# Performance work log

Measured on AMD Instinct MI355X. Metric: run time of the kernel, lower is better.

## Reference

```python
import jax, jax.numpy as jnp
import numpy as np

N, D, K = 262144, 64, 512


def setup_inputs() -> dict:
    key = jax.random.key(0)
    k1, k2 = jax.random.split(key)
    x = jax.random.normal(k1, (N, D), dtype=jnp.float32)
    # embedding initialized uniform(-1/K, 1/K) as in the torch module
    codebook = jax.random.uniform(k2, (K, D), dtype=jnp.float32, minval=-1.0 / K, maxval=1.0 / K)
    return {"x": x, "codebook": codebook}


def reference(x, codebook):
    # distances[n,k] = ||x_n||^2 + ||w_k||^2 - 2 x_n . w_k  (cdist^2 via matmul)
    d = (jnp.sum(x * x, axis=1, keepdims=True)
         + jnp.sum(codebook * codebook, axis=1)
         - 2.0 * jnp.matmul(x, codebook.T))  # [N, K]
    indices = jnp.argmin(d, axis=1)          # [N]
    x_q = codebook[indices]                  # [N, D] gather
    commitment_loss = jnp.mean((jax.lax.stop_gradient(x_q) - x) ** 2)
    embedding_loss = jnp.mean((x_q - jax.lax.stop_gradient(x)) ** 2)
    vq_loss = commitment_loss * 0.25 + embedding_loss
    # straight-through estimator
    x_out = x + jax.lax.stop_gradient(x_q - x)
    return (x_out, vq_loss)
```

## Files before the change

### kernel.cpp

```cpp
#include <hip/hip_runtime.h>
#include <hip/hip_bf16.h>

#define N_ROWS 262144
#define DIM    64
#define KCB    512

#define BLOCKS  512
#define THREADS 512

typedef __bf16 bf16x8 __attribute__((ext_vector_type(8)));
typedef float  f32x4  __attribute__((ext_vector_type(4)));

__device__ inline float dot4(float4 a) {
    return a.x * a.x + a.y * a.y + a.z * a.z + a.w * a.w;
}

__global__ void vq_wnorm(const float* __restrict__ cb, float* __restrict__ wn) {
    int k = threadIdx.x;
    if (k < KCB) {
        const float* w = cb + k * DIM;
        float s = 0.f;
        #pragma unroll
        for (int d = 0; d < DIM; ++d) s += w[d] * w[d];
        wn[k] = 1.0f + 0.5f * s;
    }
}

__global__ __launch_bounds__(THREADS, 4) void vq_main(
    const float* __restrict__ x, const float* __restrict__ cb,
    const float* __restrict__ wn, float* __restrict__ out,
    float* __restrict__ partials)
{
    __shared__ bf16x8 cb_sh[KCB * 8];
    __shared__ f32x4  wn_sh4[KCB / 4];
    __shared__ float  red_sh[THREADS];

    const int tid    = threadIdx.x;
    const int lane   = tid & 63;
    const int wave   = tid >> 6;
    const int lane15 = lane & 15;
    const int half   = lane >> 4;

    for (int fg = tid; fg < KCB * 8; fg += THREADS) {
        int row = fg >> 3, g = fg & 7;
        const float* src = cb + row * DIM + g * 8;
        float4 f0 = *(const float4*)src;
        float4 f1 = *(const float4*)(src + 4);
        bf16x8 v;
        v[0] = (__bf16)(-f0.x); v[1] = (__bf16)(-f0.y); v[2] = (__bf16)(-f0.z); v[3] = (__bf16)(-f0.w);
        v[4] = (__bf16)(-f1.x); v[5] = (__bf16)(-f1.y); v[6] = (__bf16)(-f1.z); v[7] = (__bf16)(-f1.w);
        cb_sh[row * 8 + (g ^ (row & 7))] = v;
    }
    for (int i = tid; i < KCB; i += THREADS) ((float*)wn_sh4)[i] = wn[i];

    const int wrow = blockIdx.x * (8 * 64) + wave * 64;
    bf16x8 blo[4], bhi[4];
    float  xn[4];
    #pragma unroll
    for (int c = 0; c < 4; ++c) {
        const float* xr = x + (size_t)(wrow + c * 16 + lane15) * DIM + half * 8;
        float4 f0 = *(const float4*)xr;
        float4 f1 = *(const float4*)(xr + 4);
        float4 f2 = *(const float4*)(xr + 32);
        float4 f3 = *(const float4*)(xr + 36);
        xn[c] = dot4(f0) + dot4(f1) + dot4(f2) + dot4(f3);
        bf16x8 lo, hi;
        lo[0] = (__bf16)f0.x; lo[1] = (__bf16)f0.y; lo[2] = (__bf16)f0.z; lo[3] = (__bf16)f0.w;
        lo[4] = (__bf16)f1.x; lo[5] = (__bf16)f1.y; lo[6] = (__bf16)f1.z; lo[7] = (__bf16)f1.w;
        hi[0] = (__bf16)f2.x; hi[1] = (__bf16)f2.y; hi[2] = (__bf16)f2.z; hi[3] = (__bf16)f2.w;
        hi[4] = (__bf16)f3.x; hi[5] = (__bf16)f3.y; hi[6] = (__bf16)f3.z; hi[7] = (__bf16)f3.w;
        blo[c] = lo; bhi[c] = hi;
    }
    __syncthreads();

    const int swz_lo = half ^ (lane & 7);
    const int swz_hi = (4 + half) ^ (lane & 7);
    const unsigned halfbits = (unsigned)(half * 4);

    unsigned u0 = 0xFFFFFFFFu, u1 = 0xFFFFFFFFu, u2 = 0xFFFFFFFFu, u3 = 0xFFFFFFFFu;

    #pragma unroll 8
    for (int t = 0; t < 32; ++t) {
        const int arow = t * 16 + lane15;
        bf16x8 alo = cb_sh[arow * 8 + swz_lo];
        bf16x8 ahi = cb_sh[arow * 8 + swz_hi];
        f32x4  wnv = wn_sh4[t * 4 + half];
        unsigned* us[4] = {&u0, &u1, &u2, &u3};
        #pragma unroll
        for (int c = 0; c < 4; ++c) {
            f32x4 acc = wnv;
            acc = __builtin_amdgcn_mfma_f32_16x16x32_bf16(alo, blo[c], acc, 0, 0, 0);
            acc = __builtin_amdgcn_mfma_f32_16x16x32_bf16(ahi, bhi[c], acc, 0, 0, 0);
            unsigned p0 = (__float_as_uint(acc[0]) & 0xFFFFFE00u) | (unsigned)(t * 16 + 0) | halfbits;
            unsigned p1 = (__float_as_uint(acc[1]) & 0xFFFFFE00u) | (unsigned)(t * 16 + 1) | halfbits;
            unsigned p2 = (__float_as_uint(acc[2]) & 0xFFFFFE00u) | (unsigned)(t * 16 + 2) | halfbits;
            unsigned p3 = (__float_as_uint(acc[3]) & 0xFFFFFE00u) | (unsigned)(t * 16 + 3) | halfbits;
            unsigned a = p0 < p1 ? p0 : p1;
            unsigned b = p2 < p3 ? p2 : p3;
            unsigned m = a < b ? a : b;
            *us[c] = (*us[c] < m) ? *us[c] : m;
        }
    }

    float lossAcc = 0.f;
    int bks[4];
    unsigned uc[4] = {u0, u1, u2, u3};
    #pragma unroll
    for (int c = 0; c < 4; ++c) {
        unsigned v = uc[c];
        unsigned w16 = (unsigned)__shfl_xor((int)v, 16); v = v < w16 ? v : w16;
        unsigned w32 = (unsigned)__shfl_xor((int)v, 32); v = v < w32 ? v : w32;
        float xnf = xn[c];
        xnf += __shfl_xor(xnf, 16);
        xnf += __shfl_xor(xnf, 32);
        bks[c] = (int)(v & 511u);
        float sstar = __uint_as_float(v & 0xFFFFFE00u);
        lossAcc += 0.25f * (xnf + 2.f * (sstar - 1.f));
    }

    float* outw = out + (size_t)wrow * DIM;
    #pragma unroll
    for (int j = 0; j < 16; ++j) {
        int srcl = (j * 4 + half) & 15;
        int bk   = __shfl(bks[j >> 2], srcl);
        float4 q = *(const float4*)(cb + (size_t)bk * DIM + (lane & 15) * 4);
        *(float4*)(outw + j * 256 + lane * 4) = q;
    }

    red_sh[tid] = lossAcc;
    __syncthreads();
    #pragma unroll
    for (int s = THREADS / 2; s > 0; s >>= 1) {
        if (tid < s) red_sh[tid] += red_sh[tid + s];
        __syncthreads();
    }
    if (tid == 0) partials[blockIdx.x] = red_sh[0];
}

__global__ void vq_finalize(const float* __restrict__ partials,
                            float* __restrict__ out_loss) {
    __shared__ float sh[256];
    int t = threadIdx.x;
    sh[t] = partials[t] + partials[t + 256];
    __syncthreads();
    #pragma unroll
    for (int s = 128; s > 0; s >>= 1) {
        if (t < s) sh[t] += sh[t + s];
        __syncthreads();
    }
    if (t == 0) out_loss[0] = sh[0] * (1.25f / (float)(N_ROWS * DIM));
}

extern "C" void kernel_launch(void* const* d_in, const int* in_sizes, int n_in,
                              void* d_out, int out_size, void* d_ws, size_t ws_size,
                              hipStream_t stream) {
    const float* x  = (const float*)d_in[0];
    const float* cb = (const float*)d_in[1];
    float* out      = (float*)d_out;
    float* wn       = (float*)d_ws;
    float* partials = wn + KCB;

    hipLaunchKernelGGL(vq_wnorm, dim3(1), dim3(512), 0, stream, cb, wn);
    hipLaunchKernelGGL(vq_main, dim3(BLOCKS), dim3(THREADS), 0, stream,
                       x, cb, wn, out, partials);
    hipLaunchKernelGGL(vq_finalize, dim3(1), dim3(256), 0, stream,
                       partials, out + (size_t)N_ROWS * DIM);
}
```

Baseline: 45.74 us.

## Fuse codebook norm into main kernel, double threads per block, use shuffle reductions

```diff
diff --git a/kernel.cpp b/kernel.cpp
--- a/kernel.cpp
+++ b/kernel.cpp
@@ -6,7 +6,7 @@
 #define KCB    512
 
 #define BLOCKS  512
-#define THREADS 512
+#define THREADS 1024
 
 typedef __bf16 bf16x8 __attribute__((ext_vector_type(8)));
 typedef float  f32x4  __attribute__((ext_vector_type(4)));
@@ -15,25 +15,13 @@
     return a.x * a.x + a.y * a.y + a.z * a.z + a.w * a.w;
 }
 
-__global__ void vq_wnorm(const float* __restrict__ cb, float* __restrict__ wn) {
-    int k = threadIdx.x;
-    if (k < KCB) {
-        const float* w = cb + k * DIM;
-        float s = 0.f;
-        #pragma unroll
-        for (int d = 0; d < DIM; ++d) s += w[d] * w[d];
-        wn[k] = 1.0f + 0.5f * s;
-    }
-}
-
-__global__ __launch_bounds__(THREADS, 4) void vq_main(
+__global__ __launch_bounds__(THREADS, 8) void vq_main(
     const float* __restrict__ x, const float* __restrict__ cb,
-    const float* __restrict__ wn, float* __restrict__ out,
-    float* __restrict__ partials)
+    float* __restrict__ out, float* __restrict__ partials)
 {
     __shared__ bf16x8 cb_sh[KCB * 8];
     __shared__ f32x4  wn_sh4[KCB / 4];
-    __shared__ float  red_sh[THREADS];
+    __shared__ float  red_sh[16];
 
     const int tid    = threadIdx.x;
     const int lane   = tid & 63;
@@ -41,23 +29,29 @@
     const int lane15 = lane & 15;
     const int half   = lane >> 4;
 
-    for (int fg = tid; fg < KCB * 8; fg += THREADS) {
-        int row = fg >> 3, g = fg & 7;
+    #pragma unroll
+    for (int it = 0; it < (KCB * 8) / THREADS; ++it) {
+        const int fg = tid + it * THREADS;
+        const int row = fg >> 3, g = fg & 7;
         const float* src = cb + row * DIM + g * 8;
         float4 f0 = *(const float4*)src;
         float4 f1 = *(const float4*)(src + 4);
+        float sq = dot4(f0) + dot4(f1);
+        sq += __shfl_xor(sq, 1);
+        sq += __shfl_xor(sq, 2);
+        sq += __shfl_xor(sq, 4);
         bf16x8 v;
         v[0] = (__bf16)(-f0.x); v[1] = (__bf16)(-f0.y); v[2] = (__bf16)(-f0.z); v[3] = (__bf16)(-f0.w);
         v[4] = (__bf16)(-f1.x); v[5] = (__bf16)(-f1.y); v[6] = (__bf16)(-f1.z); v[7] = (__bf16)(-f1.w);
         cb_sh[row * 8 + (g ^ (row & 7))] = v;
+        if (g == 0) ((float*)wn_sh4)[row] = 1.0f + 0.5f * sq;
     }
-    for (int i = tid; i < KCB; i += THREADS) ((float*)wn_sh4)[i] = wn[i];
 
-    const int wrow = blockIdx.x * (8 * 64) + wave * 64;
-    bf16x8 blo[4], bhi[4];
-    float  xn[4];
+    const int wrow = blockIdx.x * 512 + wave * 32;
+    bf16x8 blo[2], bhi[2];
+    float  xn[2];
     #pragma unroll
-    for (int c = 0; c < 4; ++c) {
+    for (int c = 0; c < 2; ++c) {
         const float* xr = x + (size_t)(wrow + c * 16 + lane15) * DIM + half * 8;
         float4 f0 = *(const float4*)xr;
         float4 f1 = *(const float4*)(xr + 4);
@@ -77,7 +71,7 @@
     const int swz_hi = (4 + half) ^ (lane & 7);
     const unsigned halfbits = (unsigned)(half * 4);
 
-    unsigned u0 = 0xFFFFFFFFu, u1 = 0xFFFFFFFFu, u2 = 0xFFFFFFFFu, u3 = 0xFFFFFFFFu;
+    unsigned u0 = 0xFFFFFFFFu, u1 = 0xFFFFFFFFu;
 
     #pragma unroll 8
     for (int t = 0; t < 32; ++t) {
@@ -85,9 +79,9 @@
         bf16x8 alo = cb_sh[arow * 8 + swz_lo];
         bf16x8 ahi = cb_sh[arow * 8 + swz_hi];
         f32x4  wnv = wn_sh4[t * 4 + half];
-        unsigned* us[4] = {&u0, &u1, &u2, &u3};
+        unsigned* us[2] = {&u0, &u1};
         #pragma unroll
-        for (int c = 0; c < 4; ++c) {
+        for (int c = 0; c < 2; ++c) {
             f32x4 acc = wnv;
             acc = __builtin_amdgcn_mfma_f32_16x16x32_bf16(alo, blo[c], acc, 0, 0, 0);
             acc = __builtin_amdgcn_mfma_f32_16x16x32_bf16(ahi, bhi[c], acc, 0, 0, 0);
@@ -103,10 +97,10 @@
     }
 
     float lossAcc = 0.f;
-    int bks[4];
-    unsigned uc[4] = {u0, u1, u2, u3};
+    int bks[2];
+    unsigned uc[2] = {u0, u1};
     #pragma unroll
-    for (int c = 0; c < 4; ++c) {
+    for (int c = 0; c < 2; ++c) {
         unsigned v = uc[c];
         unsigned w16 = (unsigned)__shfl_xor((int)v, 16); v = v < w16 ? v : w16;
         unsigned w32 = (unsigned)__shfl_xor((int)v, 32); v = v < w32 ? v : w32;
@@ -120,21 +114,23 @@
 
     float* outw = out + (size_t)wrow * DIM;
     #pragma unroll
-    for (int j = 0; j < 16; ++j) {
+    for (int j = 0; j < 8; ++j) {
         int srcl = (j * 4 + half) & 15;
         int bk   = __shfl(bks[j >> 2], srcl);
         float4 q = *(const float4*)(cb + (size_t)bk * DIM + (lane & 15) * 4);
         *(float4*)(outw + j * 256 + lane * 4) = q;
     }
 
-    red_sh[tid] = lossAcc;
+    #pragma unroll
+    for (int off = 1; off < 64; off <<= 1) lossAcc += __shfl_xor(lossAcc, off);
+    if (lane == 0) red_sh[wave] = lossAcc;
     __syncthreads();
-    #pragma unroll
-    for (int s = THREADS / 2; s > 0; s >>= 1) {
-        if (tid < s) red_sh[tid] += red_sh[tid + s];
-        __syncthreads();
+    if (tid < 64) {
+        float v = (lane < 16) ? red_sh[lane] : 0.f;
+        #pragma unroll
+        for (int off = 1; off < 16; off <<= 1) v += __shfl_xor(v, off);
+        if (tid == 0) partials[blockIdx.x] = v;
     }
-    if (tid == 0) partials[blockIdx.x] = red_sh[0];
 }
 
 __global__ void vq_finalize(const float* __restrict__ partials,
@@ -157,12 +153,10 @@
     const float* x  = (const float*)d_in[0];
     const float* cb = (const float*)d_in[1];
     float* out      = (float*)d_out;
-    float* wn       = (float*)d_ws;
-    float* partials = wn + KCB;
+    float* partials = (float*)d_ws;
 
-    hipLaunchKernelGGL(vq_wnorm, dim3(1), dim3(512), 0, stream, cb, wn);
     hipLaunchKernelGGL(vq_main, dim3(BLOCKS), dim3(THREADS), 0, stream,
-                       x, cb, wn, out, partials);
+                       x, cb, out, partials);
     hipLaunchKernelGGL(vq_finalize, dim3(1), dim3(256), 0, stream,
                        partials, out + (size_t)N_ROWS * DIM);
 }
```

Result: slower. 52.42 us (+14.6%).
